# Kernel optimization log

Measured on AMD Instinct MI355X. Metric: run time of the kernel, lower is better.

The kernel has to match this reference:

```python
import jax, jax.numpy as jnp
import numpy as np

IN_FEATURES = 4096
OUT_FEATURES = 4096
RANK = 32
ALPHA = 1.0
SCALE = ALPHA / RANK


def _kaiming_uniform(key, shape):
    # matches torch.nn.init.kaiming_uniform_(a=sqrt(5)) for a 2D weight:
    # gain = sqrt(2/(1+a^2)) = sqrt(1/3); bound = gain*sqrt(3/fan_in) = 1/sqrt(fan_in)
    fan_in = shape[1]  # torch fan_in of an (in_features, rank) tensor is shape[1]
    bound = 1.0 / np.sqrt(fan_in)
    return jax.random.uniform(key, shape, jnp.float32, -bound, bound)


def setup_inputs() -> dict:
    key = jax.random.key(0)
    kx, ka1, ka2, ka3 = jax.random.split(key, 4)
    x = jax.random.normal(kx, (4, 4096, IN_FEATURES), dtype=jnp.float32)
    A_fast = _kaiming_uniform(ka1, (IN_FEATURES, RANK))
    A_med = _kaiming_uniform(ka2, (IN_FEATURES, RANK))
    A_slow = _kaiming_uniform(ka3, (IN_FEATURES, RANK))
    # B matrices are zero-initialized in the module; use small random values so
    # the output is non-trivial for correctness checking.
    kb1, kb2, kb3 = jax.random.split(jax.random.fold_in(key, 7), 3)
    B_fast = 0.02 * jax.random.normal(kb1, (RANK, OUT_FEATURES), dtype=jnp.float32)
    B_med = 0.02 * jax.random.normal(kb2, (RANK, OUT_FEATURES), dtype=jnp.float32)
    B_slow = 0.02 * jax.random.normal(kb3, (RANK, OUT_FEATURES), dtype=jnp.float32)
    return {"x": x, "A_fast": A_fast, "B_fast": B_fast,
            "A_med": A_med, "B_med": B_med,
            "A_slow": A_slow, "B_slow": B_slow}


def reference(x, A_fast, B_fast, A_med, B_med, A_slow, B_slow):
    # Fused form: concat ranks -> two larger GEMMs, then scale.
    A = jnp.concatenate([A_fast, A_med, A_slow], axis=1)   # [in, 3r]
    B = jnp.concatenate([B_fast, B_med, B_slow], axis=0)   # [3r, out]
    h = jnp.einsum('bsi,ir->bsr', x, A)                    # [B, S, 3r]
    out = jnp.einsum('bsr,ro->bso', h, B) * SCALE          # [B, S, out]
    return out
```

## Files before the change

kernel.cpp:

```cpp
#include <hip/hip_runtime.h>
#include <hip/hip_bf16.h>

typedef __attribute__((ext_vector_type(4))) float f32x4;
typedef __attribute__((ext_vector_type(8))) short bf16x8;

__device__ __forceinline__ unsigned short f2bf(float f) {
  unsigned int u = __builtin_bit_cast(unsigned int, f);
  u += 0x7FFFu + ((u >> 16) & 1u);
  return (unsigned short)(u >> 16);
}

__device__ __forceinline__ void async_ld16(const void* g, void* l) {
  __builtin_amdgcn_global_load_lds(
      (__attribute__((address_space(1))) void*)g,
      (__attribute__((address_space(3))) void*)l, 16, 0, 0);
}

__global__ __launch_bounds__(256) void pack_AB(
    const float* __restrict__ Af, const float* __restrict__ Am,
    const float* __restrict__ As, const float* __restrict__ Bf,
    const float* __restrict__ Bm, const float* __restrict__ Bs,
    short* __restrict__ Apack, short* __restrict__ Bpack)
{
  unsigned idx = blockIdx.x * 256u + threadIdx.x;
  if (idx < 393216u) {
    unsigned j = idx & 7u, lane = (idx >> 3) & 63u, rest = idx >> 9;
    unsigned t = rest % 6u, chunk = rest / 6u;
    unsigned k = chunk * 32u + ((lane >> 4) << 3) + j;
    unsigned c = t * 16u + (lane & 15u);
    float v;
    if (c < 32u)      v = Af[k * 32u + c];
    else if (c < 64u) v = Am[k * 32u + (c - 32u)];
    else              v = As[k * 32u + (c - 64u)];
    Apack[idx] = (short)f2bf(v);
  } else {
    unsigned i2 = idx - 393216u;
    unsigned j = i2 & 7u, lane = (i2 >> 3) & 63u, rest = i2 >> 9;
    unsigned nt = rest & 255u, kc = rest >> 8;
    unsigned k = kc * 32u + ((lane >> 4) << 3) + j;
    unsigned n = nt * 16u + (lane & 15u);
    float v;
    if (k < 32u)      v = Bf[k * 4096u + n];
    else if (k < 64u) v = Bm[(k - 32u) * 4096u + n];
    else              v = Bs[(k - 64u) * 4096u + n];
    Bpack[i2] = (short)f2bf(v * 0.03125f);
  }
}

__global__ __launch_bounds__(256, 4) void lora_stage1(
    const float* __restrict__ x, const short* __restrict__ Apack,
    short* __restrict__ hg)
{
  const int rb  = blockIdx.x;
  const int tid = threadIdx.x;
  const int w = tid >> 6, l = tid & 63;
  const int lm = l & 15, lk = l >> 4;
  const size_t rowbase = (size_t)rb * 16;

  __shared__ __align__(16) float smem[8192];

  f32x4 acc[6];
#pragma unroll
  for (int t = 0; t < 6; ++t) acc[t] = (f32x4){0.f, 0.f, 0.f, 0.f};

  auto stage = [&](int s, int b) {
    float* base = smem + b * 4096;
    const float* gx = x + rowbase * 4096 + s * 256;
#pragma unroll
    for (int i = 0; i < 4; ++i) {
      int r = w * 4 + i;
      async_ld16(gx + (size_t)r * 4096 + ((l ^ (r & 7)) << 2), base + r * 256);
    }
  };

  auto consume = [&](int st) {
    const float* rowp = smem + (st & 1) * 4096 + lm * 256;
    const int sw = lm & 7;
#pragma unroll
    for (int p = 0; p < 2; ++p) {
      int ksub = w * 2 + p;
      int b0 = ksub * 8 + lk * 2;
      f32x4 xa = *(const f32x4*)(rowp + (((b0)     ^ sw) << 2));
      f32x4 xb = *(const f32x4*)(rowp + (((b0 + 1) ^ sw) << 2));
      bf16x8 xf;
      xf[0] = (short)f2bf(xa[0]); xf[1] = (short)f2bf(xa[1]);
      xf[2] = (short)f2bf(xa[2]); xf[3] = (short)f2bf(xa[3]);
      xf[4] = (short)f2bf(xb[0]); xf[5] = (short)f2bf(xb[1]);
      xf[6] = (short)f2bf(xb[2]); xf[7] = (short)f2bf(xb[3]);
      int kchunk = st * 8 + ksub;
#pragma unroll
      for (int t = 0; t < 6; ++t) {
        bf16x8 av = *(const bf16x8*)(Apack + ((size_t)kchunk * 6 + t) * 512 + l * 8);
        acc[t] = __builtin_amdgcn_mfma_f32_16x16x32_bf16(xf, av, acc[t], 0, 0, 0);
      }
    }
  };

  stage(0, 0);
#pragma unroll 1
  for (int st = 0; st < 15; ++st) {
    stage(st + 1, (st + 1) & 1);
    __builtin_amdgcn_sched_barrier(0);
    asm volatile("s_waitcnt vmcnt(4)" ::: "memory");
    __builtin_amdgcn_sched_barrier(0);
    __builtin_amdgcn_s_barrier();
    __builtin_amdgcn_sched_barrier(0);
    consume(st);
    __builtin_amdgcn_sched_barrier(0);
    __builtin_amdgcn_s_barrier();
    __builtin_amdgcn_sched_barrier(0);
  }
  asm volatile("s_waitcnt vmcnt(0)" ::: "memory");
  __builtin_amdgcn_sched_barrier(0);
  __builtin_amdgcn_s_barrier();
  __builtin_amdgcn_sched_barrier(0);
  consume(15);
  __syncthreads();

  {
    float* hpw = smem + w * 1600;
#pragma unroll
    for (int t = 0; t < 6; ++t)
#pragma unroll
      for (int q = 0; q < 4; ++q)
        hpw[(lk * 4 + q) * 100 + t * 16 + lm] = acc[t][q];
  }
  __syncthreads();

  if (tid < 192) {
    int r = tid / 12, c8 = tid % 12;
    const float* p = smem + r * 100 + c8 * 8;
    f32x4 s0 = *(const f32x4*)(p)        + *(const f32x4*)(p + 1600)
             + *(const f32x4*)(p + 3200) + *(const f32x4*)(p + 4800);
    f32x4 s1 = *(const f32x4*)(p + 4)    + *(const f32x4*)(p + 1604)
             + *(const f32x4*)(p + 3204) + *(const f32x4*)(p + 4804);
    bf16x8 o;
    o[0] = (short)f2bf(s0[0]); o[1] = (short)f2bf(s0[1]);
    o[2] = (short)f2bf(s0[2]); o[3] = (short)f2bf(s0[3]);
    o[4] = (short)f2bf(s1[0]); o[5] = (short)f2bf(s1[1]);
    o[6] = (short)f2bf(s1[2]); o[7] = (short)f2bf(s1[3]);
    *(bf16x8*)(hg + ((size_t)rb * 192 + (c8 >> 2) * 64 + (c8 & 3) * 16 + r) * 8) = o;
  }
}

__global__ __launch_bounds__(256, 8) void lora_stage2(
    const short* __restrict__ hg, const short* __restrict__ Bpack,
    float* __restrict__ out)
{
  const int rb = blockIdx.x >> 3;
  const int cb = blockIdx.x & 7;
  const int tid = threadIdx.x;
  const int w = tid >> 6, l = tid & 63;
  const int lm = l & 15, lk = l >> 4;
  const int tile = rb * 4 + w;

  bf16x8 hf[3];
#pragma unroll
  for (int kc = 0; kc < 3; ++kc)
    hf[kc] = *(const bf16x8*)(hg + ((size_t)tile * 192 + kc * 64 + l) * 8);

  float* orow = out + ((size_t)tile * 16 + lm) * 4096;
  const short* bp = Bpack + (size_t)l * 8;

#pragma unroll 2
  for (int i = 0; i < 32; ++i) {
    int nt = cb * 32 + i;
    f32x4 a = {0.f, 0.f, 0.f, 0.f};
#pragma unroll
    for (int kc = 0; kc < 3; ++kc) {
      bf16x8 bv = *(const bf16x8*)(bp + (size_t)(kc * 256 + nt) * 512);
      a = __builtin_amdgcn_mfma_f32_16x16x32_bf16(bv, hf[kc], a, 0, 0, 0);
    }
    *(f32x4*)(orow + nt * 16 + lk * 4) = a;
  }
}

extern "C" void kernel_launch(void* const* d_in, const int* in_sizes, int n_in,
                              void* d_out, int out_size, void* d_ws, size_t ws_size,
                              hipStream_t stream) {
  const float* x  = (const float*)d_in[0];
  const float* Af = (const float*)d_in[1];
  const float* Bf = (const float*)d_in[2];
  const float* Am = (const float*)d_in[3];
  const float* Bm = (const float*)d_in[4];
  const float* As = (const float*)d_in[5];
  const float* Bs = (const float*)d_in[6];
  float* out = (float*)d_out;

  char* ws = (char*)d_ws;
  short* Apack = (short*)ws;
  short* Bpack = (short*)(ws + 786432);
  short* hg    = (short*)(ws + 2 * 786432);

  hipLaunchKernelGGL(pack_AB, dim3(3072), dim3(256), 0, stream,
                     Af, Am, As, Bf, Bm, Bs, Apack, Bpack);
  hipLaunchKernelGGL(lora_stage1, dim3(1024), dim3(256), 0, stream, x, Apack, hg);
  hipLaunchKernelGGL(lora_stage2, dim3(2048), dim3(256), 0, stream, hg, Bpack, out);
}
```

Baseline: 155.6 us.

## Restructure LoRA stage2 to keep B fragments in registers and stream h tiles

Stage2 now has each wave hold four column tiles of packed B (12 bf16x8 fragments) in registers and loop over 8 row tiles, loading h per tile. Before, it kept h in registers and reloaded B from global memory for every column tile. Grid decomposition changes to 128 row-slabs by 16 column blocks, and the occupancy hint drops from 8 to 4 blocks. The aim is to cut repeated B loads and L2 traffic. The costs are higher register pressure and a different output write pattern, in a kernel that is dominated by writing the 256MB fp32 output.

```diff
diff --git a/kernel.cpp b/kernel.cpp
--- a/kernel.cpp
+++ b/kernel.cpp
@@ -143,35 +143,41 @@
   }
 }
 
-__global__ __launch_bounds__(256, 8) void lora_stage2(
+__global__ __launch_bounds__(256, 4) void lora_stage2(
     const short* __restrict__ hg, const short* __restrict__ Bpack,
     float* __restrict__ out)
 {
-  const int rb = blockIdx.x >> 3;
-  const int cb = blockIdx.x & 7;
+  const int bid = blockIdx.x;
+  const int rs = bid >> 4;
+  const int cb = bid & 15;
   const int tid = threadIdx.x;
   const int w = tid >> 6, l = tid & 63;
   const int lm = l & 15, lk = l >> 4;
-  const int tile = rb * 4 + w;
-
-  bf16x8 hf[3];
-#pragma unroll
-  for (int kc = 0; kc < 3; ++kc)
-    hf[kc] = *(const bf16x8*)(hg + ((size_t)tile * 192 + kc * 64 + l) * 8);
-
-  float* orow = out + ((size_t)tile * 16 + lm) * 4096;
-  const short* bp = Bpack + (size_t)l * 8;
+  const int nt0 = cb * 16 + w * 4;
+
+  bf16x8 bf[4][3];
+#pragma unroll
+  for (int n = 0; n < 4; ++n)
+#pragma unroll
+    for (int kc = 0; kc < 3; ++kc)
+      bf[n][kc] = *(const bf16x8*)(Bpack + ((size_t)(kc * 256 + nt0 + n)) * 512 + l * 8);
 
 #pragma unroll 2
-  for (int i = 0; i < 32; ++i) {
-    int nt = cb * 32 + i;
-    f32x4 a = {0.f, 0.f, 0.f, 0.f};
-#pragma unroll
-    for (int kc = 0; kc < 3; ++kc) {
-      bf16x8 bv = *(const bf16x8*)(bp + (size_t)(kc * 256 + nt) * 512);
-      a = __builtin_amdgcn_mfma_f32_16x16x32_bf16(bv, hf[kc], a, 0, 0, 0);
+  for (int it = 0; it < 8; ++it) {
+    const int tile = rs * 8 + it;
+    const short* hp = hg + (size_t)tile * 1536 + (size_t)l * 8;
+    bf16x8 hf0 = *(const bf16x8*)(hp);
+    bf16x8 hf1 = *(const bf16x8*)(hp + 512);
+    bf16x8 hf2 = *(const bf16x8*)(hp + 1024);
+    float* orow = out + ((size_t)tile * 16 + lm) * 4096;
+#pragma unroll
+    for (int n = 0; n < 4; ++n) {
+      f32x4 a = {0.f, 0.f, 0.f, 0.f};
+      a = __builtin_amdgcn_mfma_f32_16x16x32_bf16(bf[n][0], hf0, a, 0, 0, 0);
+      a = __builtin_amdgcn_mfma_f32_16x16x32_bf16(bf[n][1], hf1, a, 0, 0, 0);
+      a = __builtin_amdgcn_mfma_f32_16x16x32_bf16(bf[n][2], hf2, a, 0, 0, 0);
+      *(f32x4*)(orow + (nt0 + n) * 16 + lk * 4) = a;
     }
-    *(f32x4*)(orow + nt * 16 + lk * 4) = a;
   }
 }
 
```

Result: faster. 141.4 us (-9.1%).

## Stage stage2 output through LDS for fully coalesced row stores

Applied to the files above, without the earlier changes.

Stage2 now runs one 16-row tile per block, with the four waves splitting the output columns. Each wave writes its MFMA results into a padded LDS buffer, then reads them back so that each wave stores whole contiguous 1 KB row segments. Previously, each lane wrote 16-byte pieces scattered across 16 rows. The goal is better coalescing on the write-dominated output (256 MB of fp32), at the cost of LDS round trips, two barriers per iteration, half as many blocks, and lower occupancy bounds.

```diff
diff --git a/kernel.cpp b/kernel.cpp
--- a/kernel.cpp
+++ b/kernel.cpp
@@ -3,6 +3,8 @@
 
 typedef __attribute__((ext_vector_type(4))) float f32x4;
 typedef __attribute__((ext_vector_type(8))) short bf16x8;
+
+#define SBAR __builtin_amdgcn_sched_barrier(0)
 
 __device__ __forceinline__ unsigned short f2bf(float f) {
   unsigned int u = __builtin_bit_cast(unsigned int, f);
@@ -100,20 +102,20 @@
 #pragma unroll 1
   for (int st = 0; st < 15; ++st) {
     stage(st + 1, (st + 1) & 1);
-    __builtin_amdgcn_sched_barrier(0);
+    SBAR;
     asm volatile("s_waitcnt vmcnt(4)" ::: "memory");
-    __builtin_amdgcn_sched_barrier(0);
-    __builtin_amdgcn_s_barrier();
-    __builtin_amdgcn_sched_barrier(0);
+    SBAR;
+    __builtin_amdgcn_s_barrier();
+    SBAR;
     consume(st);
-    __builtin_amdgcn_sched_barrier(0);
-    __builtin_amdgcn_s_barrier();
-    __builtin_amdgcn_sched_barrier(0);
+    SBAR;
+    __builtin_amdgcn_s_barrier();
+    SBAR;
   }
   asm volatile("s_waitcnt vmcnt(0)" ::: "memory");
-  __builtin_amdgcn_sched_barrier(0);
+  SBAR;
   __builtin_amdgcn_s_barrier();
-  __builtin_amdgcn_sched_barrier(0);
+  SBAR;
   consume(15);
   __syncthreads();
 
@@ -143,35 +145,60 @@
   }
 }
 
-__global__ __launch_bounds__(256, 8) void lora_stage2(
+__global__ __launch_bounds__(256, 4) void lora_stage2(
     const short* __restrict__ hg, const short* __restrict__ Bpack,
     float* __restrict__ out)
 {
-  const int rb = blockIdx.x >> 3;
-  const int cb = blockIdx.x & 7;
+  const int tile = blockIdx.x;
   const int tid = threadIdx.x;
   const int w = tid >> 6, l = tid & 63;
   const int lm = l & 15, lk = l >> 4;
-  const int tile = rb * 4 + w;
+
+  __shared__ __align__(16) float trans[16 * 284];
 
   bf16x8 hf[3];
 #pragma unroll
   for (int kc = 0; kc < 3; ++kc)
-    hf[kc] = *(const bf16x8*)(hg + ((size_t)tile * 192 + kc * 64 + l) * 8);
-
-  float* orow = out + ((size_t)tile * 16 + lm) * 4096;
-  const short* bp = Bpack + (size_t)l * 8;
-
-#pragma unroll 2
-  for (int i = 0; i < 32; ++i) {
-    int nt = cb * 32 + i;
-    f32x4 a = {0.f, 0.f, 0.f, 0.f};
-#pragma unroll
-    for (int kc = 0; kc < 3; ++kc) {
-      bf16x8 bv = *(const bf16x8*)(bp + (size_t)(kc * 256 + nt) * 512);
-      a = __builtin_amdgcn_mfma_f32_16x16x32_bf16(bv, hf[kc], a, 0, 0, 0);
-    }
-    *(f32x4*)(orow + nt * 16 + lk * 4) = a;
+    hf[kc] = *(const bf16x8*)(hg + (size_t)tile * 1536 + kc * 512 + (size_t)l * 8);
+
+  const int rc   = l * 4;
+  const int rpos = rc + ((rc >> 5) << 2);
+  float* orow0 = out + (size_t)tile * 16 * 4096;
+
+#pragma unroll 1
+  for (int p = 0; p < 16; ++p) {
+    f32x4 a[4];
+#pragma unroll
+    for (int n = 0; n < 4; ++n) {
+      const int nt = p * 16 + w * 4 + n;
+      f32x4 acc = {0.f, 0.f, 0.f, 0.f};
+#pragma unroll
+      for (int kc = 0; kc < 3; ++kc) {
+        bf16x8 bv = *(const bf16x8*)(Bpack + ((size_t)(kc * 256 + nt)) * 512 + l * 8);
+        acc = __builtin_amdgcn_mfma_f32_16x16x32_bf16(bv, hf[kc], acc, 0, 0, 0);
+      }
+      a[n] = acc;
+    }
+#pragma unroll
+    for (int n = 0; n < 4; ++n) {
+      int c = (w * 4 + n) * 16 + lk * 4;
+      int pos = c + ((c >> 5) << 2);
+      *(f32x4*)&trans[lm * 284 + pos] = a[n];
+    }
+    SBAR;
+    asm volatile("s_waitcnt lgkmcnt(0)" ::: "memory");
+    SBAR;
+    __builtin_amdgcn_s_barrier();
+    SBAR;
+#pragma unroll
+    for (int rr = 0; rr < 4; ++rr) {
+      int row = w * 4 + rr;
+      f32x4 v = *(const f32x4*)&trans[row * 284 + rpos];
+      *(f32x4*)(orow0 + (size_t)row * 4096 + p * 256 + rc) = v;
+    }
+    SBAR;
+    __builtin_amdgcn_s_barrier();
+    SBAR;
   }
 }
 
@@ -195,5 +222,5 @@
   hipLaunchKernelGGL(pack_AB, dim3(3072), dim3(256), 0, stream,
                      Af, Am, As, Bf, Bm, Bs, Apack, Bpack);
   hipLaunchKernelGGL(lora_stage1, dim3(1024), dim3(256), 0, stream, x, Apack, hg);
-  hipLaunchKernelGGL(lora_stage2, dim3(2048), dim3(256), 0, stream, hg, Bpack, out);
-}
+  hipLaunchKernelGGL(lora_stage2, dim3(1024), dim3(256), 0, stream, hg, Bpack, out);
+}
```

Result: slower. 160.7 us (+3.3%).
